# Performance work log

Measured on AMD Instinct MI355X. Metric: run time of the kernel, lower is better.

## Reference

```python
import jax, jax.numpy as jnp
import numpy as np

D_MODEL = 512; N_HEADS = 8; D_HIDDEN = 512
STACK_DEPTH = 48; STACK_WIDTH = 128; D_FF = 2048; D_SS = 128
SEQ = 512; BATCH = 16
EP = 1e-4; MAX_ITER = 100


def nonsat(x):
    # fixed-point iteration y_ = (2y^3/3 + x)/(y^2+1); torch detaches y each step,
    # so grads flow only through x in the final step. Loop runs on stopped values.
    xs = jax.lax.stop_gradient(x)
    step = lambda y: (2.0 * y ** 3 / 3.0 + xs) / (y * y + 1.0)
    def cond(s):
        y, y_, i = s
        return jnp.logical_and(jnp.mean(jnp.abs(y_ - y)) > EP, i <= MAX_ITER)
    def body(s):
        y, y_, i = s
        return (y_, step(y_), i + 1)
    y_last, _, _ = jax.lax.while_loop(cond, body, (xs, step(xs), jnp.int32(0)))
    return (2.0 * y_last ** 3 / 3.0 + x) / (y_last * y_last + 1.0)


def layer_norm(x, g, b, eps=1e-5):
    m = jnp.mean(x, axis=-1, keepdims=True)
    v = jnp.mean((x - m) ** 2, axis=-1, keepdims=True)
    return (x - m) / jnp.sqrt(v + eps) * g + b


def mha(x, k_mask, wi, bi, wo, bo):
    # x: (S,B,E), torch nn.MultiheadAttention with combined in_proj, causal mask
    S, B, E = x.shape
    H = N_HEADS; hd = E // H
    qkv = x @ wi.T + bi
    q, k, v = jnp.split(qkv, 3, axis=-1)
    to_heads = lambda t: t.reshape(S, B, H, hd).transpose(1, 2, 0, 3)  # (B,H,S,hd)
    q = to_heads(q) * (hd ** -0.5)
    k = to_heads(k); v = to_heads(v)
    scores = jnp.einsum('bhqd,bhkd->bhqk', q, k)
    causal = jnp.triu(jnp.full((S, S), -jnp.inf, dtype=x.dtype), 1)
    scores = scores + causal
    scores = jnp.where(k_mask[:, None, None, :], -jnp.inf, scores)
    a = jax.nn.softmax(scores, axis=-1)
    o = jnp.einsum('bhqk,bhkd->bhqd', a, v).transpose(2, 0, 1, 3).reshape(S, B, E)
    return o @ wo.T + bo


def setup_inputs() -> dict:
    key = jax.random.key(0)
    ks = iter(jax.random.split(key, 32))
    E = D_MODEL
    def w(shape, fan_in):
        return (jax.random.normal(next(ks), shape, jnp.float32) / np.sqrt(fan_in)).astype(jnp.float32)
    inp = {
        'x_in': jax.random.normal(next(ks), (SEQ, BATCH, E), jnp.float32),
        'hidden_prev': jax.random.normal(next(ks), (BATCH, SEQ, D_HIDDEN), jnp.float32),
        'stack_prev': jax.random.normal(next(ks), (BATCH, SEQ, STACK_DEPTH, STACK_WIDTH), jnp.float32),
        'k_mask': jnp.zeros((BATCH, SEQ), dtype=bool),
        'in_proj_w': w((3 * E, E), E), 'in_proj_b': jnp.zeros((3 * E,), jnp.float32),
        'out_proj_w': w((E, E), E), 'out_proj_b': jnp.zeros((E,), jnp.float32),
        'ln1_g': jnp.ones((E,), jnp.float32), 'ln1_b': jnp.zeros((E,), jnp.float32),
        'ln2_g': jnp.ones((E,), jnp.float32), 'ln2_b': jnp.zeros((E,), jnp.float32),
        'ff_w1': w((D_FF, E), E), 'ff_b1': jnp.zeros((D_FF,), jnp.float32),
        'ff_w2': w((E, D_FF), D_FF), 'ff_b2': jnp.zeros((E,), jnp.float32),
        'W_w': w((D_HIDDEN, E), E), 'W_b': jnp.zeros((D_HIDDEN,), jnp.float32),
        'R_w': w((D_HIDDEN, D_HIDDEN), D_HIDDEN), 'R_b': jnp.zeros((D_HIDDEN,), jnp.float32),
        'P_w': w((D_HIDDEN, STACK_WIDTH), STACK_WIDTH), 'P_b': jnp.zeros((D_HIDDEN,), jnp.float32),
        'V_w': w((D_SS, E + D_HIDDEN), E + D_HIDDEN),
        'U_w': w((E, D_SS), D_SS),
        'A_w': w((3, D_HIDDEN), D_HIDDEN), 'A_b': jnp.zeros((3,), jnp.float32),
        'D_w': w((STACK_WIDTH, D_HIDDEN), D_HIDDEN), 'D_b': jnp.zeros((STACK_WIDTH,), jnp.float32),
    }
    return inp


def reference(x_in, hidden_prev, stack_prev, k_mask,
              in_proj_w, in_proj_b, out_proj_w, out_proj_b,
              ln1_g, ln1_b, ln2_g, ln2_b,
              ff_w1, ff_b1, ff_w2, ff_b2,
              W_w, W_b, R_w, R_b, P_w, P_b,
              V_w, U_w, A_w, A_b, D_w, D_b):
    # sublayer 1: pre-norm residual multihead self-attention
    x = x_in + mha(layer_norm(x_in, ln1_g, ln1_b), k_mask,
                   in_proj_w, in_proj_b, out_proj_w, out_proj_b)
    # stack-augmented memory update
    stack_x = stack_prev[:, :, 0, :]                       # (B,S,W) stack top
    xb = x.transpose(1, 0, 2)                              # (B,S,E)
    hidden = xb @ W_w.T + W_b + hidden_prev @ R_w.T + R_b + stack_x @ P_w.T + P_b
    hidden = nonsat(hidden)                                # (B,S,Dh)
    vx = jnp.concatenate([x, hidden.transpose(1, 0, 2)], axis=-1)  # (S,B,E+Dh)
    y = jax.nn.softmax(vx @ V_w.T, axis=-1) @ U_w.T        # (S,B,E)
    x = 0.5 * (x + y)
    stack_inp = nonsat(hidden @ D_w.T + D_b)[:, :, None, :]        # (B,S,1,W)
    controls = jax.nn.softmax(hidden @ A_w.T + A_b, axis=-1)       # (B,S,3)
    a_push = controls[:, :, 0, None, None]
    a_pop = controls[:, :, 1, None, None]
    a_noop = controls[:, :, 2, None, None]
    zeros_bot = jnp.zeros_like(stack_prev[:, :, :1])
    stack_down = jnp.concatenate([stack_prev[:, :, 1:], zeros_bot], axis=2)
    stack_up = jnp.concatenate([stack_inp, stack_prev[:, :, :-1]], axis=2)
    stack = a_noop * stack_prev + a_push * stack_up + a_pop * stack_down
    # sublayer 2: pre-norm residual position-wise FFN
    h = layer_norm(x, ln2_g, ln2_b)
    x = x + (jax.nn.relu(h @ ff_w1.T + ff_b1) @ ff_w2.T + ff_b2)
    return (x, hidden, stack)
```

## Files before the change

kernel.cpp:

```cpp
#include <hip/hip_runtime.h>
#include <stdint.h>

typedef unsigned short u16;
typedef short short8 __attribute__((ext_vector_type(8)));
typedef float f32x4 __attribute__((ext_vector_type(4)));

__device__ __forceinline__ u16 f2b(float f) {
    uint32_t x = __float_as_uint(f);
    uint32_t r = x + 0x7fffu + ((x >> 16) & 1u);
    return (u16)(r >> 16);
}

__device__ __forceinline__ float nonsat_f(float x) {
    float y = x;
#pragma unroll
    for (int t = 0; t < 14; ++t) {
        const float y2 = y * y;
        y = (0.66666667f * y2 * y + x) / (y2 + 1.f);
    }
    return y;
}

__device__ __forceinline__ void gl2lds16(const u16* g, u16* l) {
    __builtin_amdgcn_global_load_lds(
        (const __attribute__((address_space(1))) unsigned int*)g,
        (__attribute__((address_space(3))) unsigned int*)l, 16, 0, 0);
}

template <int MT, int MODE, bool RELU>
__global__ __launch_bounds__(256) void gemm_k(
    const u16* __restrict__ A, int lda,
    const u16* __restrict__ B, int ldb,
    const float* __restrict__ bias,
    int M, int N, int K,
    u16* __restrict__ out_b, float* __restrict__ out_f,
    const float* __restrict__ res_f, u16* __restrict__ out_b2)
{
    constexpr int MI = MT / 64;
    constexpr int WI = MT / 32;
    constexpr int ATILE = MT * 32;
    const int tn = blockIdx.x, tm = blockIdx.y;
    const int tid = threadIdx.x;
    const int wave = tid >> 6, lane = tid & 63;
    const int quad = lane >> 4, mm = lane & 15;
    const int wr = (wave >> 1) * (MT / 2), wc = (wave & 1) * 64;

    __shared__ __align__(16) u16 As[2 * ATILE];
    __shared__ __align__(16) u16 Bs[2 * 4096];

    const f32x4 vzero = {0.f, 0.f, 0.f, 0.f};
    f32x4 acc[WI][4];
#pragma unroll
    for (int i = 0; i < WI; i++)
#pragma unroll
        for (int j = 0; j < 4; j++) acc[i][j] = vzero;

    const int lr = tid >> 2;
    const int lc = (tid & 3) * 8;
    const u16* ag[MI];
#pragma unroll
    for (int h = 0; h < MI; h++)
        ag[h] = A + (size_t)(tm * MT + lr + h * 64) * lda + lc;
    const u16* bg0 = B + (size_t)(tn * 128 + lr) * ldb + lc;
    const u16* bg1 = B + (size_t)(tn * 128 + lr + 64) * ldb + lc;

    auto STAGE = [&](int s, int kt) {
#pragma unroll
        for (int h = 0; h < MI; h++)
            gl2lds16(ag[h] + kt, As + s * ATILE + h * 2048 + wave * 512);
        gl2lds16(bg0 + kt, Bs + s * 4096 + wave * 512);
        gl2lds16(bg1 + kt, Bs + s * 4096 + 2048 + wave * 512);
    };

    const int nt = K >> 5;
    STAGE(0, 0);
    asm volatile("s_waitcnt vmcnt(0)" ::: "memory");
    __syncthreads();
    int cur = 0;

    for (int t = 0; t < nt; ++t) {
        if (t + 1 < nt) STAGE(cur ^ 1, (t + 1) * 32);
        const u16* as = As + cur * ATILE;
        const u16* bs = Bs + cur * 4096;
        short8 af[WI], bfr[4];
#pragma unroll
        for (int i = 0; i < WI; i++) af[i] = *(const short8*)(as + (wr + i * 16 + mm) * 32 + quad * 8);
#pragma unroll
        for (int j = 0; j < 4; j++) bfr[j] = *(const short8*)(bs + (wc + j * 16 + mm) * 32 + quad * 8);
#pragma unroll
        for (int i = 0; i < WI; i++)
#pragma unroll
            for (int j = 0; j < 4; j++)
                acc[i][j] = __builtin_amdgcn_mfma_f32_16x16x32_bf16(af[i], bfr[j], acc[i][j], 0, 0, 0);
        if (t + 1 < nt) {
            asm volatile("s_waitcnt vmcnt(0)" ::: "memory");
            __syncthreads();
            cur ^= 1;
        }
    }

    if constexpr (MODE == 8) {
        __shared__ __align__(16) float Sm[64 * 130];
        __syncthreads();
#pragma unroll
        for (int j = 0; j < 4; j++)
#pragma unroll
            for (int i = 0; i < WI; i++)
#pragma unroll
                for (int r = 0; r < 4; r++)
                    Sm[(wr + i * 16 + quad * 4 + r) * 130 + wc + j * 16 + mm] = acc[i][j][r];
        __syncthreads();
#pragma unroll
        for (int rr = 0; rr < 16; ++rr) {
            const int row_l = wave * 16 + rr;
            const float a = Sm[row_l * 130 + lane];
            const float b = Sm[row_l * 130 + 64 + lane];
            float mx = fmaxf(a, b);
#pragma unroll
            for (int off = 1; off < 64; off <<= 1) mx = fmaxf(mx, __shfl_xor(mx, off));
            const float ea = __expf(a - mx), eb = __expf(b - mx);
            float s = ea + eb;
#pragma unroll
            for (int off = 1; off < 64; off <<= 1) s += __shfl_xor(s, off);
            const float inv = 1.f / s;
            const size_t rowg = (size_t)tm * MT + row_l;
            out_b[rowg * 128 + lane] = f2b(ea * inv);
            out_b[rowg * 128 + 64 + lane] = f2b(eb * inv);
        }
        return;
    }

#pragma unroll
    for (int j = 0; j < 4; j++) {
        const int colg = tn * 128 + wc + j * 16 + mm;
        const float bv = bias ? bias[colg] : 0.f;
#pragma unroll
        for (int i = 0; i < WI; i++) {
#pragma unroll
            for (int r = 0; r < 4; r++) {
                const int rowg = tm * MT + wr + i * 16 + quad * 4 + r;
                float v = acc[i][j][r] + bv;
                const size_t off = (size_t)rowg * N + colg;
                if constexpr (MODE == 0) {
                    if (RELU) v = fmaxf(v, 0.f);
                    out_b[off] = f2b(v);
                } else if constexpr (MODE == 3) {
                    v += res_f[off];
                    out_f[off] = v;
                    const u16 hb = f2b(v);
                    out_b[(size_t)rowg * 1024 + colg] = hb;
                    out_b2[((size_t)(rowg & 15) * 512 + (rowg >> 4)) * 1152 + colg] = hb;
                } else if constexpr (MODE == 4) {
                    v = 0.5f * (v + res_f[off]);
                    out_f[off] = v;
                } else if constexpr (MODE == 5) {
                    v += res_f[off];
                    out_f[off] = v;
                } else if constexpr (MODE == 6) {
                    v = nonsat_f(v);
                    out_f[off] = v;
                    out_b[((size_t)(rowg & 511) * 16 + (rowg >> 9)) * 1024 + 512 + colg] = f2b(v);
                } else {
                    v = nonsat_f(v);
                    out_f[off] = v;
                }
            }
        }
    }
}

struct CvtArgs {
    const float* s[12];
    unsigned cum[13];
};

static constexpr unsigned C_INPJ = 0;
static constexpr unsigned C_OUTP = 786432;
static constexpr unsigned C_FF1W = 1048576;
static constexpr unsigned C_FF2W = 2097152;
static constexpr unsigned C_WRP  = 3145728;
static constexpr unsigned C_VW   = 3735552;
static constexpr unsigned C_UW   = 3866624;
static constexpr unsigned C_DW   = 3932160;
static constexpr unsigned C_WTOT = 3997696;

__global__ __launch_bounds__(256) void cvt_k(CvtArgs a, u16* __restrict__ wa, u16* __restrict__ ha,
                                             const float* __restrict__ Wb, const float* __restrict__ Rb,
                                             const float* __restrict__ Pb, float* __restrict__ bsum)
{
    if (blockIdx.x == gridDim.x - 1) {
        if (threadIdx.x < 128) {
            const int c = threadIdx.x * 4;
#pragma unroll
            for (int k = 0; k < 4; k++) bsum[c + k] = Wb[c + k] + Rb[c + k] + Pb[c + k];
        }
        return;
    }
    const unsigned t = (blockIdx.x * 256u + threadIdx.x) * 8u;
    if (t >= a.cum[12]) return;
    int g = 0;
#pragma unroll
    for (int i = 1; i < 12; i++)
        if (t >= a.cum[i]) g = i;
    const unsigned e = t - a.cum[g];
    const float* src;
    u16* dst;
    if (g == 10) {
        src = a.s[10] + e;
        dst = ha + (size_t)(e >> 9) * 1152 + 512 + (e & 511);
    } else if (g == 11) {
        src = a.s[11] + (size_t)(e >> 7) * 6144 + (e & 127);
        dst = ha + (size_t)(e >> 7) * 1152 + 1024 + (e & 127);
    } else if (g == 4) {
        src = a.s[4] + e;
        dst = wa + C_WRP + (size_t)(e >> 9) * 1152 + (e & 511);
    } else if (g == 5) {
        src = a.s[5] + e;
        dst = wa + C_WRP + (size_t)(e >> 9) * 1152 + 512 + (e & 511);
    } else if (g == 6) {
        src = a.s[6] + e;
        dst = wa + C_WRP + (size_t)(e >> 7) * 1152 + 1024 + (e & 127);
    } else {
        src = a.s[g] + e;
        dst = wa + t;
    }
    float4 u0 = *(const float4*)src;
    float4 u1 = *(const float4*)(src + 4);
    __align__(16) u16 o[8] = {f2b(u0.x), f2b(u0.y), f2b(u0.z), f2b(u0.w),
                              f2b(u1.x), f2b(u1.y), f2b(u1.z), f2b(u1.w)};
    *(int4*)dst = *(const int4*)o;
}

__global__ __launch_bounds__(64) void attn_k(const u16* __restrict__ QKV, u16* __restrict__ O)
{
    const int qt = blockIdx.x;
    const int bh = blockIdx.y;
    const int b = bh >> 3, h = bh & 7;
    const int lane = threadIdx.x;
    const int quad = lane >> 4, mm = lane & 15;
    const int cbase = h * 64;
    const float NEGINF = -3.0e38f;

    __shared__ __align__(16) u16 Pl[64 * 72];
    __shared__ __align__(16) u16 Vl[64 * 72];

    short8 qf[4][2];
#pragma unroll
    for (int rt = 0; rt < 4; ++rt) {
        const int s = qt * 64 + rt * 16 + mm;
        const u16* p = QKV + ((size_t)s * 16 + b) * 1536 + cbase + quad * 8;
        qf[rt][0] = *(const short8*)(p);
        qf[rt][1] = *(const short8*)(p + 32);
    }

    const f32x4 vzero = {0.f, 0.f, 0.f, 0.f};
    f32x4 of[4][4];
#pragma unroll
    for (int i = 0; i < 4; i++)
#pragma unroll
        for (int j = 0; j < 4; j++) of[i][j] = vzero;
    float mrow[4][4], lrow[4][4];
#pragma unroll
    for (int i = 0; i < 4; i++)
#pragma unroll
        for (int r = 0; r < 4; r++) { mrow[i][r] = NEGINF; lrow[i][r] = 0.f; }

    for (int kt = 0; kt <= qt; ++kt) {
        short8 kf[4][2];
#pragma unroll
        for (int nt = 0; nt < 4; ++nt) {
            const int kk = kt * 64 + nt * 16 + mm;
            const u16* p = QKV + ((size_t)kk * 16 + b) * 1536 + 512 + cbase + quad * 8;
            kf[nt][0] = *(const short8*)(p);
            kf[nt][1] = *(const short8*)(p + 32);
        }
        f32x4 sf[4][4];
#pragma unroll
        for (int i = 0; i < 4; i++)
#pragma unroll
            for (int j = 0; j < 4; j++) sf[i][j] = vzero;
#pragma unroll
        for (int i = 0; i < 4; i++)
#pragma unroll
            for (int j = 0; j < 4; j++) {
                sf[i][j] = __builtin_amdgcn_mfma_f32_16x16x32_bf16(qf[i][0], kf[j][0], sf[i][j], 0, 0, 0);
                sf[i][j] = __builtin_amdgcn_mfma_f32_16x16x32_bf16(qf[i][1], kf[j][1], sf[i][j], 0, 0, 0);
            }
        {
            const int kk = lane >> 3, c8 = (lane & 7) * 8;
#pragma unroll
            for (int it = 0; it < 8; ++it) {
                const int key = kt * 64 + it * 8 + kk;
                int4 v = *(const int4*)(QKV + ((size_t)key * 16 + b) * 1536 + 1024 + cbase + c8);
                *(int4*)(Vl + (it * 8 + kk) * 72 + c8) = v;
            }
        }
        const bool diag = (kt == qt);
#pragma unroll
        for (int i = 0; i < 4; i++)
#pragma unroll
            for (int j = 0; j < 4; j++)
#pragma unroll
                for (int r = 0; r < 4; r++) {
                    float v = sf[i][j][r] * 0.125f;
                    if (diag) {
                        const int q = i * 16 + quad * 4 + r;
                        const int k = j * 16 + mm;
                        if (k > q) v = NEGINF;
                    }
                    sf[i][j][r] = v;
                }
#pragma unroll
        for (int i = 0; i < 4; i++) {
#pragma unroll
            for (int r = 0; r < 4; r++) {
                float mx = fmaxf(fmaxf(sf[i][0][r], sf[i][1][r]), fmaxf(sf[i][2][r], sf[i][3][r]));
                mx = fmaxf(mx, __shfl_xor(mx, 1));
                mx = fmaxf(mx, __shfl_xor(mx, 2));
                mx = fmaxf(mx, __shfl_xor(mx, 4));
                mx = fmaxf(mx, __shfl_xor(mx, 8));
                const float mnew = fmaxf(mrow[i][r], mx);
                const float alpha = __expf(mrow[i][r] - mnew);
                mrow[i][r] = mnew;
                float psum = 0.f;
#pragma unroll
                for (int j = 0; j < 4; j++) {
                    float p = __expf(sf[i][j][r] - mnew);
                    sf[i][j][r] = p;
                    psum += p;
                }
                psum += __shfl_xor(psum, 1);
                psum += __shfl_xor(psum, 2);
                psum += __shfl_xor(psum, 4);
                psum += __shfl_xor(psum, 8);
                lrow[i][r] = lrow[i][r] * alpha + psum;
#pragma unroll
                for (int j = 0; j < 4; j++) of[i][j][r] *= alpha;
            }
        }
#pragma unroll
        for (int i = 0; i < 4; i++)
#pragma unroll
            for (int j = 0; j < 4; j++)
#pragma unroll
                for (int r = 0; r < 4; r++)
                    Pl[(i * 16 + quad * 4 + r) * 72 + j * 16 + mm] = f2b(sf[i][j][r]);
        __syncthreads();
        short8 pa[4][2];
#pragma unroll
        for (int i = 0; i < 4; i++) {
            pa[i][0] = *(const short8*)(Pl + (i * 16 + mm) * 72 + quad * 8);
            pa[i][1] = *(const short8*)(Pl + (i * 16 + mm) * 72 + 32 + quad * 8);
        }
#pragma unroll
        for (int j = 0; j < 4; j++) {
#pragma unroll
            for (int kc = 0; kc < 2; ++kc) {
                short8 vb;
#pragma unroll
                for (int e = 0; e < 8; e++)
                    vb[e] = (short)Vl[(kc * 32 + quad * 8 + e) * 72 + j * 16 + mm];
#pragma unroll
                for (int i = 0; i < 4; i++)
                    of[i][j] = __builtin_amdgcn_mfma_f32_16x16x32_bf16(pa[i][kc], vb, of[i][j], 0, 0, 0);
            }
        }
        __syncthreads();
    }
#pragma unroll
    for (int i = 0; i < 4; i++)
#pragma unroll
        for (int r = 0; r < 4; r++) {
            const int s = qt * 64 + i * 16 + quad * 4 + r;
            const float inv = 1.f / lrow[i][r];
#pragma unroll
            for (int j = 0; j < 4; j++)
                O[((size_t)s * 16 + b) * 512 + cbase + j * 16 + mm] = f2b(of[i][j][r] * inv);
        }
}

__global__ __launch_bounds__(256) void ln_k(const float* __restrict__ x,
                                            const float* __restrict__ g,
                                            const float* __restrict__ be,
                                            u16* __restrict__ out)
{
    const int row = blockIdx.x * 4 + (threadIdx.x >> 6);
    const int lane = threadIdx.x & 63;
    const float* p = x + (size_t)row * 512 + lane * 8;
    float4 u0 = *(const float4*)p;
    float4 u1 = *(const float4*)(p + 4);
    float v[8] = {u0.x, u0.y, u0.z, u0.w, u1.x, u1.y, u1.z, u1.w};
    float s = 0.f, s2 = 0.f;
#pragma unroll
    for (int j = 0; j < 8; j++) { s += v[j]; s2 += v[j] * v[j]; }
#pragma unroll
    for (int off = 1; off < 64; off <<= 1) { s += __shfl_xor(s, off); s2 += __shfl_xor(s2, off); }
    const float mean = s * (1.f / 512.f);
    const float var = s2 * (1.f / 512.f) - mean * mean;
    const float rstd = rsqrtf(fmaxf(var, 0.f) + 1e-5f);
    float4 g0 = *(const float4*)(g + lane * 8);
    float4 g1 = *(const float4*)(g + lane * 8 + 4);
    float4 b0 = *(const float4*)(be + lane * 8);
    float4 b1 = *(const float4*)(be + lane * 8 + 4);
    const float gg[8] = {g0.x, g0.y, g0.z, g0.w, g1.x, g1.y, g1.z, g1.w};
    const float bb[8] = {b0.x, b0.y, b0.z, b0.w, b1.x, b1.y, b1.z, b1.w};
    __align__(16) u16 o[8];
#pragma unroll
    for (int j = 0; j < 8; j++)
        o[j] = f2b((v[j] - mean) * rstd * gg[j] + bb[j]);
    *(int4*)(out + (size_t)row * 512 + lane * 8) = *(const int4*)o;
}

__global__ __launch_bounds__(256) void controls_k(const float* __restrict__ H, const float* __restrict__ Aw,
                                                  const float* __restrict__ Ab, float* __restrict__ ctrl)
{
    const int row = blockIdx.x * 4 + (threadIdx.x >> 6);
    const int lane = threadIdx.x & 63;
    const float* hp = H + (size_t)row * 512 + lane * 8;
    float4 h0 = *(const float4*)hp;
    float4 h1 = *(const float4*)(hp + 4);
    const float hv[8] = {h0.x, h0.y, h0.z, h0.w, h1.x, h1.y, h1.z, h1.w};
    float d[3];
#pragma unroll
    for (int w = 0; w < 3; ++w) {
        const float* ap = Aw + w * 512 + lane * 8;
        float4 a0 = *(const float4*)ap;
        float4 a1 = *(const float4*)(ap + 4);
        const float av[8] = {a0.x, a0.y, a0.z, a0.w, a1.x, a1.y, a1.z, a1.w};
        float acc = 0.f;
#pragma unroll
        for (int j = 0; j < 8; j++) acc += hv[j] * av[j];
        d[w] = acc;
    }
#pragma unroll
    for (int off = 1; off < 64; off <<= 1) {
        d[0] += __shfl_xor(d[0], off);
        d[1] += __shfl_xor(d[1], off);
        d[2] += __shfl_xor(d[2], off);
    }
    const float l0 = d[0] + Ab[0], l1 = d[1] + Ab[1], l2 = d[2] + Ab[2];
    const float mx = fmaxf(l0, fmaxf(l1, l2));
    const float e0 = __expf(l0 - mx), e1 = __expf(l1 - mx), e2 = __expf(l2 - mx);
    const float inv = 1.f / (e0 + e1 + e2);
    if (lane == 0) {
        ctrl[(size_t)row * 3 + 0] = e0 * inv;
        ctrl[(size_t)row * 3 + 1] = e1 * inv;
        ctrl[(size_t)row * 3 + 2] = e2 * inv;
    }
}

__global__ __launch_bounds__(256) void stack_k(const float* __restrict__ sp_all, const float* __restrict__ sin,
                                               const float* __restrict__ ctrl, float* __restrict__ out)
{
    const int bs = blockIdx.x;
    const int t = blockIdx.y * 256 + threadIdx.x;
    const int d = t >> 4;
    const int w = (t & 15) * 8;
    const float* sp = sp_all + (size_t)bs * 6144;
    const float pu = ctrl[(size_t)bs * 3 + 0];
    const float po = ctrl[(size_t)bs * 3 + 1];
    const float no = ctrl[(size_t)bs * 3 + 2];
    float cur[8], up[8], dn[8];
    {
        const float* p = sp + d * 128 + w;
        float4 c0 = *(const float4*)p, c1 = *(const float4*)(p + 4);
        cur[0]=c0.x; cur[1]=c0.y; cur[2]=c0.z; cur[3]=c0.w; cur[4]=c1.x; cur[5]=c1.y; cur[6]=c1.z; cur[7]=c1.w;
    }
    {
        const int bb = bs >> 9, ss = bs & 511;
        const float* p = (d == 0) ? (sin + ((size_t)ss * 16 + bb) * 128 + w) : (sp + (d - 1) * 128 + w);
        float4 c0 = *(const float4*)p, c1 = *(const float4*)(p + 4);
        up[0]=c0.x; up[1]=c0.y; up[2]=c0.z; up[3]=c0.w; up[4]=c1.x; up[5]=c1.y; up[6]=c1.z; up[7]=c1.w;
    }
    if (d < 47) {
        const float* p = sp + (d + 1) * 128 + w;
        float4 c0 = *(const float4*)p, c1 = *(const float4*)(p + 4);
        dn[0]=c0.x; dn[1]=c0.y; dn[2]=c0.z; dn[3]=c0.w; dn[4]=c1.x; dn[5]=c1.y; dn[6]=c1.z; dn[7]=c1.w;
    } else {
#pragma unroll
        for (int j = 0; j < 8; j++) dn[j] = 0.f;
    }
    float o[8];
#pragma unroll
    for (int j = 0; j < 8; j++)
        o[j] = no * cur[j] + pu * up[j] + po * dn[j];
    float* q = out + (size_t)bs * 6144 + d * 128 + w;
    *(float4*)q = make_float4(o[0], o[1], o[2], o[3]);
    *(float4*)(q + 4) = make_float4(o[4], o[5], o[6], o[7]);
}

static constexpr size_t O_A1 = 0;
static constexpr size_t O_QKV = O_A1 + 8388608;
static constexpr size_t O_OATT = O_QKV + 25165824;
static constexpr size_t O_X1F = O_OATT + 8388608;
static constexpr size_t O_HPF = O_X1F + 16777216;
static constexpr size_t O_VL = O_HPF + 16777216;
static constexpr size_t O_X2F = O_VL + 4194304;
static constexpr size_t O_H2 = O_X2F + 16777216;
static constexpr size_t WS_NEED = O_H2 + 8388608;
static constexpr size_t O_VX = O_QKV;
static constexpr size_t O_PS = O_QKV + 16777216;
static constexpr size_t O_SIN = O_QKV + 18874368;
static constexpr size_t O_CTRL = O_QKV + 23068672;
static constexpr size_t O_FF1 = O_X1F;

static constexpr size_t WA_BYTES = (size_t)C_WTOT * 2;
static constexpr size_t HA_BYTES = (size_t)8192 * 1152 * 2;
static constexpr size_t STASH_BYTES = WA_BYTES + HA_BYTES;
static constexpr size_t STASH_OFF = 201326592 - STASH_BYTES;

extern "C" void kernel_launch(void* const* d_in, const int* in_sizes, int n_in,
                              void* d_out, int out_size, void* d_ws, size_t ws_size,
                              hipStream_t stream)
{
    (void)in_sizes; (void)n_in; (void)out_size;
    if (ws_size < WS_NEED) return;

    const float* x_in        = (const float*)d_in[0];
    const float* hidden_prev = (const float*)d_in[1];
    const float* stack_prev  = (const float*)d_in[2];
    const float* in_proj_w   = (const float*)d_in[4];
    const float* in_proj_b   = (const float*)d_in[5];
    const float* out_proj_w  = (const float*)d_in[6];
    const float* out_proj_b  = (const float*)d_in[7];
    const float* ln1_g       = (const float*)d_in[8];
    const float* ln1_b       = (const float*)d_in[9];
    const float* ln2_g       = (const float*)d_in[10];
    const float* ln2_b       = (const float*)d_in[11];
    const float* ff_w1       = (const float*)d_in[12];
    const float* ff_b1       = (const float*)d_in[13];
    const float* ff_w2       = (const float*)d_in[14];
    const float* ff_b2       = (const float*)d_in[15];
    const float* W_w         = (const float*)d_in[16];
    const float* W_b         = (const float*)d_in[17];
    const float* R_w         = (const float*)d_in[18];
    const float* R_b         = (const float*)d_in[19];
    const float* P_w         = (const float*)d_in[20];
    const float* P_b         = (const float*)d_in[21];
    const float* V_w         = (const float*)d_in[22];
    const float* U_w         = (const float*)d_in[23];
    const float* A_w         = (const float*)d_in[24];
    const float* A_b         = (const float*)d_in[25];
    const float* D_w         = (const float*)d_in[26];
    const float* D_b         = (const float*)d_in[27];

    char* ws = (char*)d_ws;
    u16* A1   = (u16*)(ws + O_A1);
    u16* QKV  = (u16*)(ws + O_QKV);
    u16* OATT = (u16*)(ws + O_OATT);
    float* X1F = (float*)(ws + O_X1F);
    float* bsum = (float*)(ws + O_VL);
    float* X2F = (float*)(ws + O_X2F);
    u16* H2   = (u16*)(ws + O_H2);
    u16* VX   = (u16*)(ws + O_VX);
    u16* PS   = (u16*)(ws + O_PS);
    float* SIN = (float*)(ws + O_SIN);
    float* CTRL = (float*)(ws + O_CTRL);
    u16* FF1  = (u16*)(ws + O_FF1);

    float* out = (float*)d_out;
    float* x_out = out;
    float* hid_out = out + 4194304;
    float* stack_out = out + 8388608;
    u16* wa = (u16*)((char*)stack_out + STASH_OFF);
    u16* ha = (u16*)((char*)wa + WA_BYTES);

    CvtArgs ca;
    ca.s[0] = in_proj_w; ca.s[1] = out_proj_w; ca.s[2] = ff_w1; ca.s[3] = ff_w2;
    ca.s[4] = W_w; ca.s[5] = R_w; ca.s[6] = P_w; ca.s[7] = V_w;
    ca.s[8] = U_w; ca.s[9] = D_w; ca.s[10] = hidden_prev; ca.s[11] = stack_prev;
    const unsigned cums[13] = {C_INPJ, C_OUTP, C_FF1W, C_FF2W, 3145728, 3407872, 3670016,
                               C_VW, C_UW, C_DW, C_WTOT, 8192000, 9240576};
    for (int i = 0; i < 13; i++) ca.cum[i] = cums[i];
    cvt_k<<<4513, 256, 0, stream>>>(ca, wa, ha, W_b, R_b, P_b, bsum);

    ln_k<<<2048, 256, 0, stream>>>(x_in, ln1_g, ln1_b, A1);
    gemm_k<128, 0, false><<<dim3(12, 64), 256, 0, stream>>>(
        A1, 512, wa + C_INPJ, 512, in_proj_b, 8192, 1536, 512, QKV, nullptr, nullptr, nullptr);
    attn_k<<<dim3(8, 128), 64, 0, stream>>>(QKV, OATT);
    gemm_k<64, 3, false><<<dim3(4, 128), 256, 0, stream>>>(
        OATT, 512, wa + C_OUTP, 512, out_proj_b, 8192, 512, 512, VX, X1F, x_in, ha);
    gemm_k<64, 6, false><<<dim3(4, 128), 256, 0, stream>>>(
        ha, 1152, wa + C_WRP, 1152, bsum, 8192, 512, 1152, VX, hid_out, nullptr, nullptr);
    gemm_k<64, 8, false><<<dim3(1, 128), 256, 0, stream>>>(
        VX, 1024, wa + C_VW, 1024, nullptr, 8192, 128, 1024, PS, nullptr, nullptr, nullptr);
    gemm_k<64, 4, false><<<dim3(4, 128), 256, 0, stream>>>(
        PS, 128, wa + C_UW, 128, nullptr, 8192, 512, 128, nullptr, X2F, X1F, nullptr);
    gemm_k<64, 7, false><<<dim3(1, 128), 256, 0, stream>>>(
        VX + 512, 1024, wa + C_DW, 512, D_b, 8192, 128, 512, nullptr, SIN, nullptr, nullptr);
    controls_k<<<2048, 256, 0, stream>>>(hid_out, A_w, A_b, CTRL);
    ln_k<<<2048, 256, 0, stream>>>(X2F, ln2_g, ln2_b, H2);
    gemm_k<128, 0, true><<<dim3(16, 64), 256, 0, stream>>>(
        H2, 512, wa + C_FF1W, 512, ff_b1, 8192, 2048, 512, FF1, nullptr, nullptr, nullptr);
    gemm_k<64, 5, false><<<dim3(4, 128), 256, 0, stream>>>(
        FF1, 2048, wa + C_FF2W, 2048, ff_b2, 8192, 512, 2048, nullptr, x_out, X2F, nullptr);
    stack_k<<<dim3(8192, 3), 256, 0, stream>>>(stack_prev, SIN, CTRL, stack_out);
}
```

Measured before the change: 728.5 us.

## Fuse controls logits into hidden GEMM, stage QKV/FF1 stores via LDS, shrink narrow-GEMM tiles

Removes the separate controls kernel. The hidden GEMM epilogue now accumulates the three A_w dot products per row, reduces them across lanes and writes them with atomicAdd into a zeroed logits buffer. The 3-way softmax moves into stack_k. The bf16-output GEMMs with 128-row tiles now stage results through LDS and write coalesced 16-byte rows. The two N=128 GEMMs use 32-row tiles to double the grid and improve occupancy. Costs are atomics, nondeterministic summation order, idle threads during A staging in the 32-row variant, and softmax recomputed per stack_k thread.

```diff
diff --git a/kernel.cpp b/kernel.cpp
--- a/kernel.cpp
+++ b/kernel.cpp
@@ -36,17 +36,23 @@
     u16* __restrict__ out_b, float* __restrict__ out_f,
     const float* __restrict__ res_f, u16* __restrict__ out_b2)
 {
-    constexpr int MI = MT / 64;
-    constexpr int WI = MT / 32;
+    constexpr int MI = (MT >= 64) ? MT / 64 : 1;
+    constexpr int WI = (MT >= 64) ? MT / 32 : 1;
     constexpr int ATILE = MT * 32;
+    constexpr size_t STAGE_B = (size_t)(2 * ATILE + 8192) * 2;
+    constexpr size_t EPIL_B = (MODE == 0 && MT == 128) ? (size_t)128 * 132 * 2
+                             : (MODE == 8 ? (size_t)MT * 130 * 4 : 0);
+    constexpr size_t SMEM_B = STAGE_B > EPIL_B ? STAGE_B : EPIL_B;
+
     const int tn = blockIdx.x, tm = blockIdx.y;
     const int tid = threadIdx.x;
     const int wave = tid >> 6, lane = tid & 63;
     const int quad = lane >> 4, mm = lane & 15;
     const int wr = (wave >> 1) * (MT / 2), wc = (wave & 1) * 64;
 
-    __shared__ __align__(16) u16 As[2 * ATILE];
-    __shared__ __align__(16) u16 Bs[2 * 4096];
+    __shared__ __align__(16) char SMEM[SMEM_B];
+    u16* As = (u16*)SMEM;
+    u16* Bs = (u16*)SMEM + 2 * ATILE;
 
     const f32x4 vzero = {0.f, 0.f, 0.f, 0.f};
     f32x4 acc[WI][4];
@@ -60,14 +66,18 @@
     const u16* ag[MI];
 #pragma unroll
     for (int h = 0; h < MI; h++)
-        ag[h] = A + (size_t)(tm * MT + lr + h * 64) * lda + lc;
+        ag[h] = A + (size_t)(tm * MT + (MT == 32 ? (lr & 31) : lr) + h * 64) * lda + lc;
     const u16* bg0 = B + (size_t)(tn * 128 + lr) * ldb + lc;
     const u16* bg1 = B + (size_t)(tn * 128 + lr + 64) * ldb + lc;
 
     auto STAGE = [&](int s, int kt) {
-#pragma unroll
-        for (int h = 0; h < MI; h++)
-            gl2lds16(ag[h] + kt, As + s * ATILE + h * 2048 + wave * 512);
+        if constexpr (MT == 32) {
+            if (tid < 128) gl2lds16(ag[0] + kt, As + s * ATILE + wave * 512);
+        } else {
+#pragma unroll
+            for (int h = 0; h < MI; h++)
+                gl2lds16(ag[h] + kt, As + s * ATILE + h * 2048 + wave * 512);
+        }
         gl2lds16(bg0 + kt, Bs + s * 4096 + wave * 512);
         gl2lds16(bg1 + kt, Bs + s * 4096 + 2048 + wave * 512);
     };
@@ -99,9 +109,35 @@
         }
     }
 
+    if constexpr (MODE == 0 && MT == 128) {
+        __syncthreads();
+        u16* Ct = (u16*)SMEM;
+#pragma unroll
+        for (int j = 0; j < 4; j++) {
+            const int colg = tn * 128 + wc + j * 16 + mm;
+            const float bv = bias ? bias[colg] : 0.f;
+#pragma unroll
+            for (int i = 0; i < WI; i++)
+#pragma unroll
+                for (int r = 0; r < 4; r++) {
+                    float v = acc[i][j][r] + bv;
+                    if (RELU) v = fmaxf(v, 0.f);
+                    Ct[(wr + i * 16 + quad * 4 + r) * 132 + wc + j * 16 + mm] = f2b(v);
+                }
+        }
+        __syncthreads();
+        const int row = tid >> 1, half = tid & 1;
+        const u16* src = Ct + row * 132 + half * 64;
+        u16* dst = out_b + (size_t)(tm * 128 + row) * N + tn * 128 + half * 64;
+#pragma unroll
+        for (int c = 0; c < 8; c++)
+            *(int4*)(dst + c * 8) = *(const int4*)(src + c * 8);
+        return;
+    }
+
     if constexpr (MODE == 8) {
-        __shared__ __align__(16) float Sm[64 * 130];
         __syncthreads();
+        float* Sm = (float*)SMEM;
 #pragma unroll
         for (int j = 0; j < 4; j++)
 #pragma unroll
@@ -111,8 +147,8 @@
                     Sm[(wr + i * 16 + quad * 4 + r) * 130 + wc + j * 16 + mm] = acc[i][j][r];
         __syncthreads();
 #pragma unroll
-        for (int rr = 0; rr < 16; ++rr) {
-            const int row_l = wave * 16 + rr;
+        for (int rr = 0; rr < MT / 4; ++rr) {
+            const int row_l = wave * (MT / 4) + rr;
             const float a = Sm[row_l * 130 + lane];
             const float b = Sm[row_l * 130 + 64 + lane];
             float mx = fmaxf(a, b);
@@ -130,10 +166,24 @@
         return;
     }
 
+    float dotp[3][WI * 4];
+    if constexpr (MODE == 6) {
+#pragma unroll
+        for (int w = 0; w < 3; w++)
+#pragma unroll
+            for (int q = 0; q < WI * 4; q++) dotp[w][q] = 0.f;
+    }
+
 #pragma unroll
     for (int j = 0; j < 4; j++) {
         const int colg = tn * 128 + wc + j * 16 + mm;
         const float bv = bias ? bias[colg] : 0.f;
+        float aw0, aw1, aw2;
+        if constexpr (MODE == 6) {
+            aw0 = res_f[colg];
+            aw1 = res_f[512 + colg];
+            aw2 = res_f[1024 + colg];
+        }
 #pragma unroll
         for (int i = 0; i < WI; i++) {
 #pragma unroll
@@ -160,12 +210,35 @@
                     v = nonsat_f(v);
                     out_f[off] = v;
                     out_b[((size_t)(rowg & 511) * 16 + (rowg >> 9)) * 1024 + 512 + colg] = f2b(v);
+                    dotp[0][i * 4 + r] += v * aw0;
+                    dotp[1][i * 4 + r] += v * aw1;
+                    dotp[2][i * 4 + r] += v * aw2;
                 } else {
                     v = nonsat_f(v);
                     out_f[off] = v;
                 }
             }
         }
+    }
+
+    if constexpr (MODE == 6) {
+        float* lg = (float*)out_b2;
+#pragma unroll
+        for (int w = 0; w < 3; w++)
+#pragma unroll
+            for (int i = 0; i < WI; i++)
+#pragma unroll
+                for (int r = 0; r < 4; r++) {
+                    float v = dotp[w][i * 4 + r];
+                    v += __shfl_xor(v, 1);
+                    v += __shfl_xor(v, 2);
+                    v += __shfl_xor(v, 4);
+                    v += __shfl_xor(v, 8);
+                    if (mm == 0) {
+                        const int rowg = tm * MT + wr + i * 16 + quad * 4 + r;
+                        atomicAdd(&lg[(size_t)rowg * 3 + w], v);
+                    }
+                }
     }
 }
 
@@ -186,7 +259,8 @@
 
 __global__ __launch_bounds__(256) void cvt_k(CvtArgs a, u16* __restrict__ wa, u16* __restrict__ ha,
                                              const float* __restrict__ Wb, const float* __restrict__ Rb,
-                                             const float* __restrict__ Pb, float* __restrict__ bsum)
+                                             const float* __restrict__ Pb, float* __restrict__ bsum,
+                                             float* __restrict__ logz)
 {
     if (blockIdx.x == gridDim.x - 1) {
         if (threadIdx.x < 128) {
@@ -194,6 +268,12 @@
 #pragma unroll
             for (int k = 0; k < 4; k++) bsum[c + k] = Wb[c + k] + Rb[c + k] + Pb[c + k];
         }
+        return;
+    }
+    if (blockIdx.x == gridDim.x - 2) {
+        float4 z = make_float4(0.f, 0.f, 0.f, 0.f);
+        float4* p = (float4*)logz;
+        for (int i = threadIdx.x; i < 6144; i += 256) p[i] = z;
         return;
     }
     const unsigned t = (blockIdx.x * 256u + threadIdx.x) * 8u;
@@ -411,55 +491,24 @@
     *(int4*)(out + (size_t)row * 512 + lane * 8) = *(const int4*)o;
 }
 
-__global__ __launch_bounds__(256) void controls_k(const float* __restrict__ H, const float* __restrict__ Aw,
-                                                  const float* __restrict__ Ab, float* __restrict__ ctrl)
-{
-    const int row = blockIdx.x * 4 + (threadIdx.x >> 6);
-    const int lane = threadIdx.x & 63;
-    const float* hp = H + (size_t)row * 512 + lane * 8;
-    float4 h0 = *(const float4*)hp;
-    float4 h1 = *(const float4*)(hp + 4);
-    const float hv[8] = {h0.x, h0.y, h0.z, h0.w, h1.x, h1.y, h1.z, h1.w};
-    float d[3];
-#pragma unroll
-    for (int w = 0; w < 3; ++w) {
-        const float* ap = Aw + w * 512 + lane * 8;
-        float4 a0 = *(const float4*)ap;
-        float4 a1 = *(const float4*)(ap + 4);
-        const float av[8] = {a0.x, a0.y, a0.z, a0.w, a1.x, a1.y, a1.z, a1.w};
-        float acc = 0.f;
-#pragma unroll
-        for (int j = 0; j < 8; j++) acc += hv[j] * av[j];
-        d[w] = acc;
-    }
-#pragma unroll
-    for (int off = 1; off < 64; off <<= 1) {
-        d[0] += __shfl_xor(d[0], off);
-        d[1] += __shfl_xor(d[1], off);
-        d[2] += __shfl_xor(d[2], off);
-    }
-    const float l0 = d[0] + Ab[0], l1 = d[1] + Ab[1], l2 = d[2] + Ab[2];
-    const float mx = fmaxf(l0, fmaxf(l1, l2));
-    const float e0 = __expf(l0 - mx), e1 = __expf(l1 - mx), e2 = __expf(l2 - mx);
-    const float inv = 1.f / (e0 + e1 + e2);
-    if (lane == 0) {
-        ctrl[(size_t)row * 3 + 0] = e0 * inv;
-        ctrl[(size_t)row * 3 + 1] = e1 * inv;
-        ctrl[(size_t)row * 3 + 2] = e2 * inv;
-    }
-}
-
 __global__ __launch_bounds__(256) void stack_k(const float* __restrict__ sp_all, const float* __restrict__ sin,
-                                               const float* __restrict__ ctrl, float* __restrict__ out)
+                                               const float* __restrict__ lg, const float* __restrict__ Ab,
+                                               float* __restrict__ out)
 {
     const int bs = blockIdx.x;
     const int t = blockIdx.y * 256 + threadIdx.x;
     const int d = t >> 4;
     const int w = (t & 15) * 8;
     const float* sp = sp_all + (size_t)bs * 6144;
-    const float pu = ctrl[(size_t)bs * 3 + 0];
-    const float po = ctrl[(size_t)bs * 3 + 1];
-    const float no = ctrl[(size_t)bs * 3 + 2];
+    const float l0 = lg[(size_t)bs * 3 + 0] + Ab[0];
+    const float l1 = lg[(size_t)bs * 3 + 1] + Ab[1];
+    const float l2 = lg[(size_t)bs * 3 + 2] + Ab[2];
+    const float mx = fmaxf(l0, fmaxf(l1, l2));
+    const float e0 = __expf(l0 - mx), e1 = __expf(l1 - mx), e2 = __expf(l2 - mx);
+    const float inv = 1.f / (e0 + e1 + e2);
+    const float pu = e0 * inv;
+    const float po = e1 * inv;
+    const float no = e2 * inv;
     float cur[8], up[8], dn[8];
     {
         const float* p = sp + d * 128 + w;
@@ -501,7 +550,7 @@
 static constexpr size_t O_VX = O_QKV;
 static constexpr size_t O_PS = O_QKV + 16777216;
 static constexpr size_t O_SIN = O_QKV + 18874368;
-static constexpr size_t O_CTRL = O_QKV + 23068672;
+static constexpr size_t O_LG = O_VL + 4096;
 static constexpr size_t O_FF1 = O_X1F;
 
 static constexpr size_t WA_BYTES = (size_t)C_WTOT * 2;
@@ -550,12 +599,12 @@
     u16* OATT = (u16*)(ws + O_OATT);
     float* X1F = (float*)(ws + O_X1F);
     float* bsum = (float*)(ws + O_VL);
+    float* LG  = (float*)(ws + O_LG);
     float* X2F = (float*)(ws + O_X2F);
     u16* H2   = (u16*)(ws + O_H2);
     u16* VX   = (u16*)(ws + O_VX);
     u16* PS   = (u16*)(ws + O_PS);
     float* SIN = (float*)(ws + O_SIN);
-    float* CTRL = (float*)(ws + O_CTRL);
     u16* FF1  = (u16*)(ws + O_FF1);
 
     float* out = (float*)d_out;
@@ -572,7 +621,7 @@
     const unsigned cums[13] = {C_INPJ, C_OUTP, C_FF1W, C_FF2W, 3145728, 3407872, 3670016,
                                C_VW, C_UW, C_DW, C_WTOT, 8192000, 9240576};
     for (int i = 0; i < 13; i++) ca.cum[i] = cums[i];
-    cvt_k<<<4513, 256, 0, stream>>>(ca, wa, ha, W_b, R_b, P_b, bsum);
+    cvt_k<<<4514, 256, 0, stream>>>(ca, wa, ha, W_b, R_b, P_b, bsum, LG);
 
     ln_k<<<2048, 256, 0, stream>>>(x_in, ln1_g, ln1_b, A1);
     gemm_k<128, 0, false><<<dim3(12, 64), 256, 0, stream>>>(
@@ -581,18 +630,17 @@
     gemm_k<64, 3, false><<<dim3(4, 128), 256, 0, stream>>>(
         OATT, 512, wa + C_OUTP, 512, out_proj_b, 8192, 512, 512, VX, X1F, x_in, ha);
     gemm_k<64, 6, false><<<dim3(4, 128), 256, 0, stream>>>(
-        ha, 1152, wa + C_WRP, 1152, bsum, 8192, 512, 1152, VX, hid_out, nullptr, nullptr);
-    gemm_k<64, 8, false><<<dim3(1, 128), 256, 0, stream>>>(
+        ha, 1152, wa + C_WRP, 1152, bsum, 8192, 512, 1152, VX, hid_out, A_w, (u16*)LG);
+    gemm_k<32, 8, false><<<dim3(1, 256), 256, 0, stream>>>(
         VX, 1024, wa + C_VW, 1024, nullptr, 8192, 128, 1024, PS, nullptr, nullptr, nullptr);
     gemm_k<64, 4, false><<<dim3(4, 128), 256, 0, stream>>>(
         PS, 128, wa + C_UW, 128, nullptr, 8192, 512, 128, nullptr, X2F, X1F, nullptr);
-    gemm_k<64, 7, false><<<dim3(1, 128), 256, 0, stream>>>(
+    gemm_k<32, 7, false><<<dim3(1, 256), 256, 0, stream>>>(
         VX + 512, 1024, wa + C_DW, 512, D_b, 8192, 128, 512, nullptr, SIN, nullptr, nullptr);
-    controls_k<<<2048, 256, 0, stream>>>(hid_out, A_w, A_b, CTRL);
     ln_k<<<2048, 256, 0, stream>>>(X2F, ln2_g, ln2_b, H2);
     gemm_k<128, 0, true><<<dim3(16, 64), 256, 0, stream>>>(
         H2, 512, wa + C_FF1W, 512, ff_b1, 8192, 2048, 512, FF1, nullptr, nullptr, nullptr);
     gemm_k<64, 5, false><<<dim3(4, 128), 256, 0, stream>>>(
         FF1, 2048, wa + C_FF2W, 2048, ff_b2, 8192, 512, 2048, nullptr, x_out, X2F, nullptr);
-    stack_k<<<dim3(8192, 3), 256, 0, stream>>>(stack_prev, SIN, CTRL, stack_out);
-}
+    stack_k<<<dim3(8192, 3), 256, 0, stream>>>(stack_prev, SIN, LG, A_b, stack_out);
+}
```

Result: no change. 718.4 us (-1.4%).
